# Kernel tuning notes

Hardware: AMD Instinct MI355X
Metric: run time of the kernel (lower is better)

## Reference

```python
import jax, jax.numpy as jnp
import numpy as np

PATCH = 3
ALPHA = 0.1


def unfold_patches(x, patch):
    """Equivalent of F.unfold(x, patch, padding=patch//2, stride=1).
    x: [B, C, H, W] -> [B, C*patch*patch, H*W].
    Note: the exact ordering of the patch-channel axis does not affect the
    downstream correlation matrix (it is summed over), so we use a simple
    shifted-view stacking.
    """
    B, C, H, W = x.shape
    p = patch // 2
    xp = jnp.pad(x, ((0, 0), (0, 0), (p, p), (p, p)))  # zero pad, like unfold
    views = [xp[:, :, i:i + H, j:j + W] for i in range(patch) for j in range(patch)]
    lf = jnp.concatenate(views, axis=1)  # [B, C*patch^2, H, W]
    return lf.reshape(B, C * patch * patch, H * W)


def setup_inputs() -> dict:
    key = jax.random.key(0)
    k1, k2 = jax.random.split(key)
    x_lab = jax.random.normal(k1, (4, 3, 64, 64), dtype=jnp.float32)
    feature = jax.random.normal(k2, (4, 64, 64, 64), dtype=jnp.float32)
    return {"x_lab": x_lab, "feature": feature}


def reference(x_lab, feature):
    # scale_factor=1 and feature already at (H, W): the torch interpolates are identity.
    B, _, H, W = x_lab.shape
    HW = H * W
    # ab channels as values: [B, HW, 2]
    x_ab = x_lab[:, 1:3].reshape(B, 2, HW).transpose(0, 2, 1)
    # local patch features: [B, C*9, HW]
    lf = unfold_patches(feature, PATCH)
    # full non-local correlation: [B, HW, HW]
    corr = jnp.einsum('bcm,bcn->bmn', lf, lf)
    attn = jax.nn.softmax(corr / ALPHA, axis=-1)
    # weighted average of ab values: [B, HW, 2]
    weighted_ab = jnp.einsum('bmn,bnc->bmc', attn, x_ab)
    return weighted_ab.transpose(0, 2, 1).reshape(B, 2, H, W)
```

## Files before the change

### kernel.cpp

```cpp
#include <hip/hip_runtime.h>
#include <math.h>


#define B_ 4
#define CH 64
#define H_ 64
#define W_ 64
#define SCALE2 14.426950408889634f
#define STRIPE 1056
#define ROWB (4 * STRIPE)
#define NRING 6

typedef __attribute__((ext_vector_type(4)))  unsigned int uint4v;
typedef __attribute__((ext_vector_type(16))) float f32x16;
typedef __attribute__((ext_vector_type(8)))  int int8v;

__device__ inline void glds16(const void* g, void* l) {
    __builtin_amdgcn_global_load_lds(
        (const __attribute__((address_space(1))) unsigned int*)g,
        (__attribute__((address_space(3))) unsigned int*)l, 16, 0, 0);
}

__device__ inline float dec_e4m3(unsigned u) {
    unsigned e = (u >> 3) & 15u, m = u & 7u;
    float v = e ? __uint_as_float(((e + 120u) << 23) | (m << 20))
                : (float)m * 0x1p-9f;
    return (u & 0x80u) ? -v : v;
}

__global__ __launch_bounds__(256) void feat_to_fp8(
    const float* __restrict__ feat, unsigned char* __restrict__ tf,
    float* __restrict__ n2)
{
    const int b = blockIdx.y, y = blockIdx.x, t = (int)threadIdx.x;
    __shared__ float ld[CH][W_ + 1];
    #pragma unroll
    for (int i = 0; i < 16; ++i) {
        int idx = i * 256 + t;
        int c = idx >> 6, x = idx & 63;
        ld[c][x] = feat[(((size_t)b * CH + c) * H_ + y) * W_ + x];
    }
    __syncthreads();
    const int x = t >> 2, g = t & 3;
    const int cbase = (g >> 1) * 32 + (g & 1) * 8;
    unsigned int wd[4];
    #pragma unroll
    for (int w4 = 0; w4 < 4; ++w4) {
        float f[4];
        #pragma unroll
        for (int e = 0; e < 4; ++e) {
            int j = w4 * 4 + e;
            f[e] = ld[cbase + ((j >> 3) << 4) + (j & 7)][x];
        }
        unsigned int wv = 0;
        wv = __builtin_amdgcn_cvt_pk_fp8_f32(f[0], f[1], wv, false);
        wv = __builtin_amdgcn_cvt_pk_fp8_f32(f[2], f[3], wv, true);
        wd[w4] = wv;
    }
    float s = 0.f;
    #pragma unroll
    for (int w4 = 0; w4 < 4; ++w4)
        #pragma unroll
        for (int e = 0; e < 4; ++e) {
            float d = dec_e4m3((wd[w4] >> (8 * e)) & 0xffu);
            s = fmaf(d, d, s);
        }
    s += __shfl_xor(s, 1);
    s += __shfl_xor(s, 2);
    if (g == 0) n2[((size_t)b * H_ + y) * W_ + x] = s;

    unsigned char* dst = tf + (((size_t)b * H_ + y) * W_ + x) * CH + g * 16;
    *(uint4v*)dst = (uint4v){wd[0], wd[1], wd[2], wd[3]};
}

#define MXMFMA(A, Bv, C) \
    __builtin_amdgcn_mfma_scale_f32_32x32x64_f8f6f4(A, Bv, C, 0, 0, 0, 0x7F, 0, 0x7F)

__global__ __launch_bounds__(512) void nlwa_fp8(
    const float* __restrict__ xlab,
    const unsigned char* __restrict__ tf,
    const float* __restrict__ n2,
    float* __restrict__ out)
{
    const int b = blockIdx.y, ym = blockIdx.x;
    const int tid = (int)threadIdx.x;
    const int w = tid >> 6, l = tid & 63;
    const int l31 = l & 31, h = l >> 5;
    const int zh = w >> 2;
    const int w4 = w & 3;
    const int mt = (w >> 1) & 1, nh = w & 1;
    const int lo = zh << 5;

    __shared__ __attribute__((aligned(16))) char smem[15 * ROWB];
    __shared__ float state[2][2][64][4];
    __shared__ float mref_lds[64];
    char* ring  = smem + zh * (NRING * ROWB);
    char* aslab = smem + 2 * NRING * ROWB;

    const unsigned char* tfb = tf + (size_t)b * H_ * W_ * CH;
    const float* aab = xlab + ((size_t)b * 3 + 1) * H_ * W_;
    const float* bab = xlab + ((size_t)b * 3 + 2) * H_ * W_;

    if (tid < 120) {
        int s15 = tid >> 3, rem = tid & 7;
        int which = rem >> 2, t = rem & 3;
        char* base = smem + s15 * ROWB;
        *(uint4v*)(base + t * STRIPE + (which ? 65 * 16 : 0)) = (uint4v){0,0,0,0};
    }
    #pragma unroll
    for (int i = 0; i < 2; ++i) ((float*)state)[i * 512 + tid] = 0.f;

    if (tid < 64) {
        const float* n2b = n2 + (size_t)b * H_ * W_;
        float s = 0.f;
        #pragma unroll
        for (int dy = -1; dy <= 1; ++dy) {
            int y = ym + dy;
            if ((unsigned)y < H_) {
                #pragma unroll
                for (int dx = -1; dx <= 1; ++dx) {
                    int x = tid + dx;
                    if ((unsigned)x < W_) s += n2b[y * W_ + x];
                }
            }
        }
        mref_lds[tid] = s * SCALE2;
    }

    auto stage = [&](char* slabBase, int y, int t) {
        char* dst = slabBase + t * STRIPE + 16;
        if ((unsigned)y < H_) {
            const unsigned char* gp = tfb + ((size_t)y * W_ + l) * CH + t * 16;
            glds16(gp, dst);
        } else {
            *(uint4v*)(dst + l * 16) = (uint4v){0, 0, 0, 0};
        }
    };

    if (zh == 0) {
        for (int tau = w4; tau < 28; tau += 4) {
            int r = tau >> 2, t = tau & 3;
            if (r < 4) {
                int y = lo - 1 + r;
                stage(ring + ((y + 1) % NRING) * ROWB, y, t);
            } else {
                int dy = r - 4;
                stage(aslab + dy * ROWB, ym + dy - 1, t);
            }
        }
    } else {
        for (int tau = w4; tau < 16; tau += 4) {
            int r = tau >> 2, t = tau & 3;
            int y = lo - 1 + r;
            stage(ring + ((y + 1) % NRING) * ROWB, y, t);
        }
    }

    const int xn = (nh << 5) + l31;
    const int xm = (mt << 5) + l31;
    const int soL = h * STRIPE;
    const int soH = (2 + h) * STRIPE;

    auto ld32 = [&](const char* slab, int off) -> int8v {
        uint4v r0 = *(const uint4v*)(slab + soL + off);
        uint4v r1 = *(const uint4v*)(slab + soH + off);
        int8v a;
        a[0] = r0[0]; a[1] = r0[1]; a[2] = r0[2]; a[3] = r0[3];
        a[4] = r1[0]; a[5] = r1[1]; a[6] = r1[2]; a[7] = r1[3];
        return a;
    };

    __syncthreads();

    int8v Areg0[3], Areg1[3], Areg2[3];
    #pragma unroll
    for (int dx = 0; dx < 3; ++dx) {
        const int oa = (xm + dx) * 16;
        Areg0[dx] = ld32(aslab + 0 * ROWB, oa);
        Areg1[dx] = ld32(aslab + 1 * ROWB, oa);
        Areg2[dx] = ld32(aslab + 2 * ROWB, oa);
    }

    float Mref[16];
    #pragma unroll
    for (int r = 0; r < 16; ++r)
        Mref[r] = mref_lds[(mt << 5) + (r & 3) + ((r >> 2) << 3) + (h << 2)];

    #pragma unroll 1
    for (int p = 0; p < 16; ++p) {
        const int y0 = lo + (p << 1);

        if (p < 15) {
            #pragma unroll
            for (int k = 0; k < 2; ++k) {
                int tau = (k << 2) + w4;
                int ri = tau >> 2, t = tau & 3;
                int y = y0 + 3 + ri;
                stage(ring + ((y + 1) % NRING) * ROWB, y, t);
            }
        }

        f32x16 acc0, acc1;
        #pragma unroll
        for (int r = 0; r < 16; ++r) { acc0[r] = 0.f; acc1[r] = 0.f; }

        const char* rb[4];
        #pragma unroll
        for (int j2 = 0; j2 < 4; ++j2)
            rb[j2] = ring + ((y0 + j2) % NRING) * ROWB;

        #pragma unroll
        for (int dx = 0; dx < 3; ++dx) {
            const int ob = (xn + dx) * 16;
            int8v Bb0 = ld32(rb[0], ob);
            int8v Bb1 = ld32(rb[1], ob);
            int8v Bb2 = ld32(rb[2], ob);
            int8v Bb3 = ld32(rb[3], ob);
            acc0 = MXMFMA(Areg0[dx], Bb0, acc0);
            acc0 = MXMFMA(Areg1[dx], Bb1, acc0);
            acc0 = MXMFMA(Areg2[dx], Bb2, acc0);
            acc1 = MXMFMA(Areg0[dx], Bb1, acc1);
            acc1 = MXMFMA(Areg1[dx], Bb2, acc1);
            acc1 = MXMFMA(Areg2[dx], Bb3, acc1);
        }

        #pragma unroll
        for (int j = 0; j < 2; ++j) {
            const f32x16& ac = (j == 0) ? acc0 : acc1;
            float v[16]; int upd = 0;
            #pragma unroll
            for (int r = 0; r < 16; ++r) {
                v[r] = fmaf(ac[r], SCALE2, -Mref[r]);
                upd |= (v[r] > -30.0f) ? 1 : 0;
            }
            if (__any(upd)) {
                const int yn = y0 + j;
                float av = aab[yn * W_ + xn];
                float bv = bab[yn * W_ + xn];
                #pragma unroll
                for (int r = 0; r < 16; ++r) {
                    float pp  = exp2f(fminf(v[r], 80.0f));
                    float w0c = pp * av;
                    float w1c = pp * bv;
                    #pragma unroll
                    for (int off = 16; off >= 1; off >>= 1) {
                        pp  += __shfl_xor(pp,  off);
                        w0c += __shfl_xor(w0c, off);
                        w1c += __shfl_xor(w1c, off);
                    }
                    if (l31 == 0) {
                        int m = (mt << 5) + (r & 3) + ((r >> 2) << 3) + (h << 2);
                        float* st = &state[zh][nh][m][0];
                        st[0] += pp; st[1] += w0c; st[2] += w1c;
                    }
                }
            }
        }
        __syncthreads();
    }

    if (tid < 64) {
        float Ssum = 0.f, w0 = 0.f, w1 = 0.f;
        #pragma unroll
        for (int z2 = 0; z2 < 2; ++z2)
            #pragma unroll
            for (int n2i = 0; n2i < 2; ++n2i) {
                Ssum += state[z2][n2i][tid][0];
                w0   += state[z2][n2i][tid][1];
                w1   += state[z2][n2i][tid][2];
            }
        float inv = 1.0f / Ssum;
        out[(((size_t)b * 2 + 0) * H_ + ym) * W_ + tid] = w0 * inv;
        out[(((size_t)b * 2 + 1) * H_ + ym) * W_ + tid] = w1 * inv;
    }
}

extern "C" void kernel_launch(void* const* d_in, const int* in_sizes, int n_in,
                              void* d_out, int out_size, void* d_ws, size_t ws_size,
                              hipStream_t stream) {
    const float* xlab = (const float*)d_in[0];
    const float* feat = (const float*)d_in[1];
    float* out = (float*)d_out;
    unsigned char* tf = (unsigned char*)d_ws;
    float* n2   = (float*)((char*)d_ws + (size_t)1024 * 1024);

    dim3 gridT(H_, B_);
    feat_to_fp8<<<gridT, 256, 0, stream>>>(feat, tf, n2);
    dim3 gridM(H_, B_);
    nlwa_fp8<<<gridM, 512, 0, stream>>>(xlab, tf, n2, out);
}
```

Before: 46.86 us.

## Process four key rows per iteration with a deeper LDS ring buffer

Each loop iteration now covers four key rows instead of two, keeping four MFMA accumulators and rotating the B operand registers so each loaded row feeds up to three accumulators. This halves the number of loop iterations and __syncthreads barriers and reduces redundant LDS loads per output row. The ring buffer grows from 6 to 10 rows to stage four rows ahead, which raises LDS use and register pressure and could reduce occupancy. The skip test also changes to a per-lane max before recomputing the logits.

Measured after the change: 49.34 us. 1.05x slower.

```diff
diff --git a/kernel.cpp b/kernel.cpp
--- a/kernel.cpp
+++ b/kernel.cpp
@@ -9,7 +9,7 @@
 #define SCALE2 14.426950408889634f
 #define STRIPE 1056
 #define ROWB (4 * STRIPE)
-#define NRING 6
+#define NRING 10
 
 typedef __attribute__((ext_vector_type(4)))  unsigned int uint4v;
 typedef __attribute__((ext_vector_type(16))) float f32x16;
@@ -91,7 +91,7 @@
     const int mt = (w >> 1) & 1, nh = w & 1;
     const int lo = zh << 5;
 
-    __shared__ __attribute__((aligned(16))) char smem[15 * ROWB];
+    __shared__ __attribute__((aligned(16))) char smem[23 * ROWB];
     __shared__ float state[2][2][64][4];
     __shared__ float mref_lds[64];
     char* ring  = smem + zh * (NRING * ROWB);
@@ -101,10 +101,10 @@
     const float* aab = xlab + ((size_t)b * 3 + 1) * H_ * W_;
     const float* bab = xlab + ((size_t)b * 3 + 2) * H_ * W_;
 
-    if (tid < 120) {
-        int s15 = tid >> 3, rem = tid & 7;
+    if (tid < 184) {
+        int s23 = tid >> 3, rem = tid & 7;
         int which = rem >> 2, t = rem & 3;
-        char* base = smem + s15 * ROWB;
+        char* base = smem + s23 * ROWB;
         *(uint4v*)(base + t * STRIPE + (which ? 65 * 16 : 0)) = (uint4v){0,0,0,0};
     }
     #pragma unroll
@@ -138,18 +138,18 @@
     };
 
     if (zh == 0) {
-        for (int tau = w4; tau < 28; tau += 4) {
+        for (int tau = w4; tau < 36; tau += 4) {
             int r = tau >> 2, t = tau & 3;
-            if (r < 4) {
+            if (r < 6) {
                 int y = lo - 1 + r;
                 stage(ring + ((y + 1) % NRING) * ROWB, y, t);
             } else {
-                int dy = r - 4;
+                int dy = r - 6;
                 stage(aslab + dy * ROWB, ym + dy - 1, t);
             }
         }
     } else {
-        for (int tau = w4; tau < 16; tau += 4) {
+        for (int tau = w4; tau < 24; tau += 4) {
             int r = tau >> 2, t = tau & 3;
             int y = lo - 1 + r;
             stage(ring + ((y + 1) % NRING) * ROWB, y, t);
@@ -187,59 +187,66 @@
         Mref[r] = mref_lds[(mt << 5) + (r & 3) + ((r >> 2) << 3) + (h << 2)];
 
     #pragma unroll 1
-    for (int p = 0; p < 16; ++p) {
-        const int y0 = lo + (p << 1);
-
-        if (p < 15) {
+    for (int p = 0; p < 8; ++p) {
+        const int y0 = lo + (p << 2);
+
+        if (p < 7) {
             #pragma unroll
-            for (int k = 0; k < 2; ++k) {
-                int tau = (k << 2) + w4;
-                int ri = tau >> 2, t = tau & 3;
-                int y = y0 + 3 + ri;
-                stage(ring + ((y + 1) % NRING) * ROWB, y, t);
-            }
-        }
-
-        f32x16 acc0, acc1;
-        #pragma unroll
-        for (int r = 0; r < 16; ++r) { acc0[r] = 0.f; acc1[r] = 0.f; }
-
-        const char* rb[4];
-        #pragma unroll
-        for (int j2 = 0; j2 < 4; ++j2)
+            for (int k = 0; k < 4; ++k) {
+                int y = y0 + 5 + k;
+                stage(ring + ((y + 1) % NRING) * ROWB, y, w4);
+            }
+        }
+
+        f32x16 acc0, acc1, acc2, acc3;
+        #pragma unroll
+        for (int r = 0; r < 16; ++r)
+            { acc0[r] = 0.f; acc1[r] = 0.f; acc2[r] = 0.f; acc3[r] = 0.f; }
+
+        const char* rb[6];
+        #pragma unroll
+        for (int j2 = 0; j2 < 6; ++j2)
             rb[j2] = ring + ((y0 + j2) % NRING) * ROWB;
 
         #pragma unroll
         for (int dx = 0; dx < 3; ++dx) {
             const int ob = (xn + dx) * 16;
-            int8v Bb0 = ld32(rb[0], ob);
-            int8v Bb1 = ld32(rb[1], ob);
-            int8v Bb2 = ld32(rb[2], ob);
-            int8v Bb3 = ld32(rb[3], ob);
-            acc0 = MXMFMA(Areg0[dx], Bb0, acc0);
-            acc0 = MXMFMA(Areg1[dx], Bb1, acc0);
-            acc0 = MXMFMA(Areg2[dx], Bb2, acc0);
-            acc1 = MXMFMA(Areg0[dx], Bb1, acc1);
-            acc1 = MXMFMA(Areg1[dx], Bb2, acc1);
-            acc1 = MXMFMA(Areg2[dx], Bb3, acc1);
-        }
-
-        #pragma unroll
-        for (int j = 0; j < 2; ++j) {
-            const f32x16& ac = (j == 0) ? acc0 : acc1;
-            float v[16]; int upd = 0;
+            int8v R0 = ld32(rb[0], ob);
+            int8v R1 = ld32(rb[1], ob);
+            int8v R2 = ld32(rb[2], ob);
+            acc0 = MXMFMA(Areg0[dx], R0, acc0);
+            acc0 = MXMFMA(Areg1[dx], R1, acc0);
+            acc0 = MXMFMA(Areg2[dx], R2, acc0);
+            R0 = ld32(rb[3], ob);
+            acc1 = MXMFMA(Areg0[dx], R1, acc1);
+            acc1 = MXMFMA(Areg1[dx], R2, acc1);
+            acc1 = MXMFMA(Areg2[dx], R0, acc1);
+            R1 = ld32(rb[4], ob);
+            acc2 = MXMFMA(Areg0[dx], R2, acc2);
+            acc2 = MXMFMA(Areg1[dx], R0, acc2);
+            acc2 = MXMFMA(Areg2[dx], R1, acc2);
+            R2 = ld32(rb[5], ob);
+            acc3 = MXMFMA(Areg0[dx], R0, acc3);
+            acc3 = MXMFMA(Areg1[dx], R1, acc3);
+            acc3 = MXMFMA(Areg2[dx], R2, acc3);
+        }
+
+        #pragma unroll
+        for (int j = 0; j < 4; ++j) {
+            const f32x16& ac = (j == 0) ? acc0 : (j == 1) ? acc1
+                             : (j == 2) ? acc2 : acc3;
+            float mx = -1e30f;
             #pragma unroll
-            for (int r = 0; r < 16; ++r) {
-                v[r] = fmaf(ac[r], SCALE2, -Mref[r]);
-                upd |= (v[r] > -30.0f) ? 1 : 0;
-            }
-            if (__any(upd)) {
+            for (int r = 0; r < 16; ++r)
+                mx = fmaxf(mx, fmaf(ac[r], SCALE2, -Mref[r]));
+            if (__any(mx > -30.0f)) {
                 const int yn = y0 + j;
                 float av = aab[yn * W_ + xn];
                 float bv = bab[yn * W_ + xn];
                 #pragma unroll
                 for (int r = 0; r < 16; ++r) {
-                    float pp  = exp2f(fminf(v[r], 80.0f));
+                    float v  = fmaf(ac[r], SCALE2, -Mref[r]);
+                    float pp  = exp2f(fminf(v, 80.0f));
                     float w0c = pp * av;
                     float w1c = pp * bv;
                     #pragma unroll
```
